# Performance work log

Measured on AMD Instinct MI355X. Metric: run time of the kernel, lower is better.

## Reference

```python
import jax, jax.numpy as jnp
import numpy as np


def _edt(fg):
    """Exact 2D Euclidean distance transform.

    fg: [B, H, W] bool, True = foreground. Returns, for every pixel, the
    Euclidean distance to the nearest background (False) pixel; 0 on
    background pixels. Matches scipy.ndimage.distance_transform_edt.
    Two-pass separable algorithm: exact 1D city-block distance along axis 1,
    then exact lower-envelope min along axis 2 via a scan over columns.
    """
    B, H, W = fg.shape
    BIG = jnp.float32(H + W)  # larger than any achievable distance
    bg = ~fg
    row_idx = jnp.arange(H, dtype=jnp.float32)[None, :, None]  # [1,H,1]

    def dist_to_prev_bg(bg_mask):
        # distance (along axis 1) to the most recent background pixel above
        last = jax.lax.cummax(jnp.where(bg_mask, row_idx, -BIG), axis=1)
        return row_idx - last

    d_up = dist_to_prev_bg(bg)
    d_down = jnp.flip(dist_to_prev_bg(jnp.flip(bg, axis=1)), axis=1)
    g = jnp.minimum(jnp.minimum(d_up, d_down), BIG)  # [B,H,W] 1D vertical dist
    g2 = g * g

    # Second pass: D2[b,h,x] = min_{x'} g2[b,h,x'] + (x - x')^2  (exact EDT^2)
    x = jnp.arange(W, dtype=jnp.float32)  # [W]

    def body(D2, inp):
        xp, g2col = inp  # scalar, [B,H]
        cand = g2col[:, :, None] + (x - xp) ** 2  # [B,H,W]
        return jnp.minimum(D2, cand), None

    D2_init = jnp.full((B, H, W), (2.0 * BIG) ** 2, dtype=jnp.float32)
    D2, _ = jax.lax.scan(body, D2_init, (x, jnp.moveaxis(g2, 2, 0)))
    return jnp.sqrt(D2)


def setup_inputs() -> dict:
    key = jax.random.key(0)
    k1, k2 = jax.random.split(key)
    B, C, H, W = 8, 4, 256, 256
    logits = jax.random.normal(k1, (B, C, H, W), dtype=jnp.float32)
    pred_softmax = jax.nn.softmax(logits, axis=1)
    mask = jax.random.randint(k2, (B, H, W), 0, C, dtype=jnp.int64)
    return {"pred_softmax": pred_softmax, "mask": mask}


def reference(pred_softmax, mask):
    B, C, H, W = pred_softmax.shape
    norm = np.float32(np.sqrt(H * H + W * W) + 1e-6)
    loss = jnp.float32(0.0)
    for c in range(1, C):  # small fixed number of classes
        fg = mask == c
        dist = _edt(fg) / norm  # [B,H,W]; all-zeros when class absent, as in ref
        loss = loss + jnp.mean(pred_softmax[:, c] * dist)
    return loss / max(C - 1, 1)
```

## Files before the change

### kernel.cpp

```cpp
#include <hip/hip_runtime.h>
#include <math.h>

#define B_    8
#define C_    4
#define H_    256
#define W_    256
#define NCLS  3
#define NROWS (NCLS * B_ * H_)
#define BIGVAL (1 << 26)

__global__ __launch_bounds__(256) void vert_g_kernel(const int* __restrict__ mask,
                                                     unsigned short* __restrict__ gbuf) {
    const int lane = threadIdx.x & 63;
    const int hc   = threadIdx.x >> 6;
    const int blk  = blockIdx.x;
    const int wt   = blk & 3;
    const int b    = (blk >> 2) & 7;
    const int c_i  = blk >> 5;
    const int cls  = c_i + 1;
    const int w    = (wt << 6) + lane;

    __shared__ int last_sh[4][64];
    __shared__ int first_sh[4][64];

    const int* mptr = mask + (b << 16) + (hc << 14) + w;
    int m[64];
    #pragma unroll
    for (int i = 0; i < 64; ++i) m[i] = mptr[i << 8];
    unsigned long long bg = 0ull;
    #pragma unroll
    for (int i = 0; i < 64; ++i)
        bg |= (unsigned long long)(m[i] != cls) << i;

    last_sh[hc][lane]  = bg ? ((hc << 6) + 63 - __builtin_clzll(bg)) : -512;
    first_sh[hc][lane] = bg ? ((hc << 6) + __builtin_ctzll(bg)) : (1 << 20);
    __syncthreads();

    int carry_up = -512;
    #pragma unroll
    for (int k = 0; k < 4; ++k)
        if (k < hc) carry_up = max(carry_up, last_sh[k][lane]);
    int carry_dn = 1 << 20;
    #pragma unroll
    for (int k = 0; k < 4; ++k)
        if (k > hc) carry_dn = min(carry_dn, first_sh[k][lane]);

    unsigned short* gout = gbuf + (((c_i << 3) + b) << 16) + (hc << 14) + w;
    #pragma unroll 4
    for (int i = 0; i < 64; ++i) {
        int h = (hc << 6) + i;
        unsigned long long le = bg & (~0ull >> (63 - i));
        int last = le ? ((hc << 6) + 63 - __builtin_clzll(le)) : carry_up;
        int du = h - last;
        unsigned long long ge = bg >> i;
        int first = ge ? (h + __builtin_ctzll(ge)) : carry_dn;
        int dd = first - h;
        int g = min(min(du, dd), 512);
        gout[i << 8] = (unsigned short)g;
    }
}

__global__ __launch_bounds__(256) void horiz_kernel(const unsigned short* __restrict__ gbuf,
                                                    const float* __restrict__ pred,
                                                    double* __restrict__ acc) {
    const int lane = threadIdx.x & 63;
    const int wv   = threadIdx.x >> 6;
    const int row  = blockIdx.x * 4 + wv;
    const int c_i  = row >> 11;
    const int b    = (row >> 8) & 7;
    const int h    = row & 255;
    const int cls  = c_i + 1;

    __shared__ __align__(16) int ext[4][512];

    const int x0 = lane << 2;
    const float* prow = pred + ((((b << 2) + cls) << 8) + h) * 256;
    float4 pv = *(const float4*)(prow + x0);
    ushort4 gv = *(const ushort4*)(gbuf + row * 256 + x0);

    int g0 = gv.x, g1 = gv.y, g2v = gv.z, g3 = gv.w;
    int q0 = g0 * g0, q1 = g1 * g1, q2 = g2v * g2v, q3 = g3 * g3;
    *(int4*)&ext[wv][128 + x0] = make_int4(q0, q1, q2, q3);
    ext[wv][lane]       = BIGVAL;
    ext[wv][64 + lane]  = BIGVAL;
    ext[wv][384 + lane] = BIGVAL;
    ext[wv][448 + lane] = BIGVAL;

    int gm = max(max(g0, g1), max(g2v, g3));
    #pragma unroll
    for (int off = 32; off > 0; off >>= 1) gm = max(gm, __shfl_xor(gm, off, 64));
    const int R = gm - 1;

    int D2[4] = { q0, q1, q2, q3 };
    const int* e = &ext[wv][128];

    if (R >= 120) {
        for (int xp = 0; xp < 256; ++xp) {
            int s = e[xp];
            #pragma unroll
            for (int j = 0; j < 4; ++j) {
                int d = (x0 + j) - xp;
                int cand = s + d * d;
                D2[j] = (cand < D2[j]) ? cand : D2[j];
            }
        }
    } else if (R >= 1) {
        for (int o = 1; o <= R; ++o) {
            int oo = o * o;
            #pragma unroll
            for (int j = 0; j < 4; ++j) {
                int xj = x0 + j;
                int c1 = e[xj + o];
                int c2 = e[xj - o];
                int cm = (c1 < c2) ? c1 : c2;
                int cand = cm + oo;
                D2[j] = (cand < D2[j]) ? cand : D2[j];
            }
        }
    }

    double sum = (double)(sqrtf((float)D2[0]) * pv.x)
               + (double)(sqrtf((float)D2[1]) * pv.y)
               + (double)(sqrtf((float)D2[2]) * pv.z)
               + (double)(sqrtf((float)D2[3]) * pv.w);
    #pragma unroll
    for (int off = 32; off > 0; off >>= 1) sum += __shfl_xor(sum, off, 64);
    if (lane == 0) acc[row] = sum;
}

__global__ __launch_bounds__(256) void final_kernel(const double* __restrict__ acc,
                                                    float* __restrict__ out) {
    const int t = threadIdx.x;
    __shared__ double wsum[4];
    double s = 0.0;
    #pragma unroll
    for (int i = 0; i < NROWS / 256; ++i) s += acc[t + i * 256];
    #pragma unroll
    for (int off = 32; off > 0; off >>= 1) s += __shfl_xor(s, off, 64);
    if ((t & 63) == 0) wsum[t >> 6] = s;
    __syncthreads();
    if (t == 0) {
        double total = wsum[0] + wsum[1] + wsum[2] + wsum[3];
        double nd = sqrt(131072.0) + 1e-6;
        double norm = (double)(float)nd;
        out[0] = (float)(total / norm / ((double)NCLS * (double)(B_ * H_ * W_)));
    }
}

extern "C" void kernel_launch(void* const* d_in, const int* in_sizes, int n_in,
                              void* d_out, int out_size, void* d_ws, size_t ws_size,
                              hipStream_t stream) {
    const float* pred = (const float*)d_in[0];
    const int*   mask = (const int*)d_in[1];
    float* out = (float*)d_out;

    char* ws = (char*)d_ws;
    double* acc = (double*)ws;
    unsigned short* gbuf = (unsigned short*)(ws + 65536);

    vert_g_kernel<<<NCLS * 8 * 4, 256, 0, stream>>>(mask, gbuf);
    horiz_kernel<<<NROWS / 4, 256, 0, stream>>>(gbuf, pred, acc);
    final_kernel<<<1, 256, 0, stream>>>(acc, out);
}
```

Measured before the change: 68.31 us.

## Fuse three kernels into one cooperative kernel with grid-wide syncs

Replaces the vertical-pass, horizontal-pass and final-reduction kernels with a single cooperative launch of 96 blocks, separated by grid.sync(). This removes two kernel launch gaps. The horizontal pass no longer uses 1536 blocks with one row per wave; each wave now processes 16 rows in batches with prefetched loads. The trade-off is far fewer waves on the GPU (384 waves), so latency hiding and parallelism for the horizontal stage are reduced, and grid.sync adds its own cost.

```diff
diff --git a/kernel.cpp b/kernel.cpp
--- a/kernel.cpp
+++ b/kernel.cpp
@@ -1,149 +1,172 @@
 #include <hip/hip_runtime.h>
+#include <hip/hip_cooperative_groups.h>
 #include <math.h>
+
+namespace cg = cooperative_groups;
 
 #define B_    8
 #define C_    4
 #define H_    256
 #define W_    256
 #define NCLS  3
-#define NROWS (NCLS * B_ * H_)
+#define NBLKC 96
 #define BIGVAL (1 << 26)
 
-__global__ __launch_bounds__(256) void vert_g_kernel(const int* __restrict__ mask,
-                                                     unsigned short* __restrict__ gbuf) {
-    const int lane = threadIdx.x & 63;
-    const int hc   = threadIdx.x >> 6;
+__global__ __launch_bounds__(256) void fused_coop(const int* __restrict__ mask,
+                                                  const float* __restrict__ pred,
+                                                  unsigned short* __restrict__ gbuf,
+                                                  double* __restrict__ part,
+                                                  float* __restrict__ out) {
+    cg::grid_group grid = cg::this_grid();
+    const int t    = threadIdx.x;
+    const int lane = t & 63;
+    const int wv   = t >> 6;
     const int blk  = blockIdx.x;
-    const int wt   = blk & 3;
-    const int b    = (blk >> 2) & 7;
-    const int c_i  = blk >> 5;
-    const int cls  = c_i + 1;
-    const int w    = (wt << 6) + lane;
 
     __shared__ int last_sh[4][64];
     __shared__ int first_sh[4][64];
+    __shared__ __align__(16) int ext[4][512];
+    __shared__ double bsum[4];
 
-    const int* mptr = mask + (b << 16) + (hc << 14) + w;
-    int m[64];
-    #pragma unroll
-    for (int i = 0; i < 64; ++i) m[i] = mptr[i << 8];
-    unsigned long long bg = 0ull;
-    #pragma unroll
-    for (int i = 0; i < 64; ++i)
-        bg |= (unsigned long long)(m[i] != cls) << i;
+    {
+        const int hc  = wv;
+        const int wt  = blk & 3;
+        const int b   = (blk >> 2) & 7;
+        const int c_i = blk >> 5;
+        const int cls = c_i + 1;
+        const int w   = (wt << 6) + lane;
 
-    last_sh[hc][lane]  = bg ? ((hc << 6) + 63 - __builtin_clzll(bg)) : -512;
-    first_sh[hc][lane] = bg ? ((hc << 6) + __builtin_ctzll(bg)) : (1 << 20);
-    __syncthreads();
+        const int* mptr = mask + (b << 16) + (hc << 14) + w;
+        int m[64];
+        #pragma unroll
+        for (int i = 0; i < 64; ++i) m[i] = mptr[i << 8];
+        unsigned long long bg = 0ull;
+        #pragma unroll
+        for (int i = 0; i < 64; ++i)
+            bg |= (unsigned long long)(m[i] != cls) << i;
 
-    int carry_up = -512;
-    #pragma unroll
-    for (int k = 0; k < 4; ++k)
-        if (k < hc) carry_up = max(carry_up, last_sh[k][lane]);
-    int carry_dn = 1 << 20;
-    #pragma unroll
-    for (int k = 0; k < 4; ++k)
-        if (k > hc) carry_dn = min(carry_dn, first_sh[k][lane]);
+        last_sh[hc][lane]  = bg ? ((hc << 6) + 63 - __builtin_clzll(bg)) : -512;
+        first_sh[hc][lane] = bg ? ((hc << 6) + __builtin_ctzll(bg)) : (1 << 20);
+        __syncthreads();
 
-    unsigned short* gout = gbuf + (((c_i << 3) + b) << 16) + (hc << 14) + w;
-    #pragma unroll 4
-    for (int i = 0; i < 64; ++i) {
-        int h = (hc << 6) + i;
-        unsigned long long le = bg & (~0ull >> (63 - i));
-        int last = le ? ((hc << 6) + 63 - __builtin_clzll(le)) : carry_up;
-        int du = h - last;
-        unsigned long long ge = bg >> i;
-        int first = ge ? (h + __builtin_ctzll(ge)) : carry_dn;
-        int dd = first - h;
-        int g = min(min(du, dd), 512);
-        gout[i << 8] = (unsigned short)g;
-    }
-}
+        int carry_up = -512;
+        #pragma unroll
+        for (int k = 0; k < 4; ++k)
+            if (k < hc) carry_up = max(carry_up, last_sh[k][lane]);
+        int carry_dn = 1 << 20;
+        #pragma unroll
+        for (int k = 0; k < 4; ++k)
+            if (k > hc) carry_dn = min(carry_dn, first_sh[k][lane]);
 
-__global__ __launch_bounds__(256) void horiz_kernel(const unsigned short* __restrict__ gbuf,
-                                                    const float* __restrict__ pred,
-                                                    double* __restrict__ acc) {
-    const int lane = threadIdx.x & 63;
-    const int wv   = threadIdx.x >> 6;
-    const int row  = blockIdx.x * 4 + wv;
-    const int c_i  = row >> 11;
-    const int b    = (row >> 8) & 7;
-    const int h    = row & 255;
-    const int cls  = c_i + 1;
-
-    __shared__ __align__(16) int ext[4][512];
-
-    const int x0 = lane << 2;
-    const float* prow = pred + ((((b << 2) + cls) << 8) + h) * 256;
-    float4 pv = *(const float4*)(prow + x0);
-    ushort4 gv = *(const ushort4*)(gbuf + row * 256 + x0);
-
-    int g0 = gv.x, g1 = gv.y, g2v = gv.z, g3 = gv.w;
-    int q0 = g0 * g0, q1 = g1 * g1, q2 = g2v * g2v, q3 = g3 * g3;
-    *(int4*)&ext[wv][128 + x0] = make_int4(q0, q1, q2, q3);
-    ext[wv][lane]       = BIGVAL;
-    ext[wv][64 + lane]  = BIGVAL;
-    ext[wv][384 + lane] = BIGVAL;
-    ext[wv][448 + lane] = BIGVAL;
-
-    int gm = max(max(g0, g1), max(g2v, g3));
-    #pragma unroll
-    for (int off = 32; off > 0; off >>= 1) gm = max(gm, __shfl_xor(gm, off, 64));
-    const int R = gm - 1;
-
-    int D2[4] = { q0, q1, q2, q3 };
-    const int* e = &ext[wv][128];
-
-    if (R >= 120) {
-        for (int xp = 0; xp < 256; ++xp) {
-            int s = e[xp];
-            #pragma unroll
-            for (int j = 0; j < 4; ++j) {
-                int d = (x0 + j) - xp;
-                int cand = s + d * d;
-                D2[j] = (cand < D2[j]) ? cand : D2[j];
-            }
-        }
-    } else if (R >= 1) {
-        for (int o = 1; o <= R; ++o) {
-            int oo = o * o;
-            #pragma unroll
-            for (int j = 0; j < 4; ++j) {
-                int xj = x0 + j;
-                int c1 = e[xj + o];
-                int c2 = e[xj - o];
-                int cm = (c1 < c2) ? c1 : c2;
-                int cand = cm + oo;
-                D2[j] = (cand < D2[j]) ? cand : D2[j];
-            }
+        unsigned short* gout = gbuf + (((c_i << 3) + b) << 16) + (hc << 14) + w;
+        #pragma unroll 4
+        for (int i = 0; i < 64; ++i) {
+            int h = (hc << 6) + i;
+            unsigned long long le = bg & (~0ull >> (63 - i));
+            int last = le ? ((hc << 6) + 63 - __builtin_clzll(le)) : carry_up;
+            int du = h - last;
+            unsigned long long ge = bg >> i;
+            int first = ge ? (h + __builtin_ctzll(ge)) : carry_dn;
+            int dd = first - h;
+            int g = min(min(du, dd), 512);
+            gout[i << 8] = (unsigned short)g;
         }
     }
 
-    double sum = (double)(sqrtf((float)D2[0]) * pv.x)
-               + (double)(sqrtf((float)D2[1]) * pv.y)
-               + (double)(sqrtf((float)D2[2]) * pv.z)
-               + (double)(sqrtf((float)D2[3]) * pv.w);
-    #pragma unroll
-    for (int off = 32; off > 0; off >>= 1) sum += __shfl_xor(sum, off, 64);
-    if (lane == 0) acc[row] = sum;
-}
+    grid.sync();
 
-__global__ __launch_bounds__(256) void final_kernel(const double* __restrict__ acc,
-                                                    float* __restrict__ out) {
-    const int t = threadIdx.x;
-    __shared__ double wsum[4];
-    double s = 0.0;
-    #pragma unroll
-    for (int i = 0; i < NROWS / 256; ++i) s += acc[t + i * 256];
-    #pragma unroll
-    for (int off = 32; off > 0; off >>= 1) s += __shfl_xor(s, off, 64);
-    if ((t & 63) == 0) wsum[t >> 6] = s;
-    __syncthreads();
-    if (t == 0) {
-        double total = wsum[0] + wsum[1] + wsum[2] + wsum[3];
-        double nd = sqrt(131072.0) + 1e-6;
-        double norm = (double)(float)nd;
-        out[0] = (float)(total / norm / ((double)NCLS * (double)(B_ * H_ * W_)));
+    double sum = 0.0;
+    {
+        ext[wv][lane]       = BIGVAL;
+        ext[wv][64 + lane]  = BIGVAL;
+        ext[wv][384 + lane] = BIGVAL;
+        ext[wv][448 + lane] = BIGVAL;
+
+        const int gi  = blk * 4 + wv;
+        const int c_i = gi >> 7;
+        const int b   = (gi >> 4) & 7;
+        const int h0  = (gi & 15) << 4;
+        const int cls = c_i + 1;
+        const int x0  = lane << 2;
+
+        const unsigned short* grow = gbuf + (((c_i << 3) + b) << 16) + (h0 << 8) + x0;
+        const float*          prow = pred + (((b << 2) + cls) << 16) + (h0 << 8) + x0;
+
+        #pragma unroll 1
+        for (int batch = 0; batch < 2; ++batch) {
+            ushort4 gv[8];
+            float4  pv[8];
+            #pragma unroll
+            for (int rr = 0; rr < 8; ++rr) {
+                int ro = ((batch << 3) + rr) << 8;
+                gv[rr] = *(const ushort4*)(grow + ro);
+                pv[rr] = *(const float4*)(prow + ro);
+            }
+            #pragma unroll 1
+            for (int rr = 0; rr < 8; ++rr) {
+                int g0 = gv[rr].x, g1 = gv[rr].y, g2v = gv[rr].z, g3 = gv[rr].w;
+                int q0 = g0 * g0, q1 = g1 * g1, q2 = g2v * g2v, q3 = g3 * g3;
+                *(int4*)&ext[wv][128 + x0] = make_int4(q0, q1, q2, q3);
+
+                int gm = max(max(g0, g1), max(g2v, g3));
+                #pragma unroll
+                for (int off = 32; off > 0; off >>= 1)
+                    gm = max(gm, __shfl_xor(gm, off, 64));
+                const int R = gm - 1;
+
+                int D2[4] = { q0, q1, q2, q3 };
+                const int* e = &ext[wv][128];
+
+                if (R >= 120) {
+                    for (int xp = 0; xp < 256; ++xp) {
+                        int s = e[xp];
+                        #pragma unroll
+                        for (int j = 0; j < 4; ++j) {
+                            int d = (x0 + j) - xp;
+                            int cand = s + d * d;
+                            D2[j] = (cand < D2[j]) ? cand : D2[j];
+                        }
+                    }
+                } else if (R >= 1) {
+                    for (int o = 1; o <= R; ++o) {
+                        int oo = o * o;
+                        #pragma unroll
+                        for (int j = 0; j < 4; ++j) {
+                            int xj = x0 + j;
+                            int c1 = e[xj + o];
+                            int c2 = e[xj - o];
+                            int cm = (c1 < c2) ? c1 : c2;
+                            int cand = cm + oo;
+                            D2[j] = (cand < D2[j]) ? cand : D2[j];
+                        }
+                    }
+                }
+
+                sum += (double)(sqrtf((float)D2[0]) * pv[rr].x)
+                     + (double)(sqrtf((float)D2[1]) * pv[rr].y)
+                     + (double)(sqrtf((float)D2[2]) * pv[rr].z)
+                     + (double)(sqrtf((float)D2[3]) * pv[rr].w);
+            }
+        }
+        #pragma unroll
+        for (int off = 32; off > 0; off >>= 1) sum += __shfl_xor(sum, off, 64);
+        if (lane == 0) part[gi] = sum;
+    }
+
+    grid.sync();
+
+    if (blk == 0) {
+        double s = part[t] + ((t < 128) ? part[t + 256] : 0.0);
+        #pragma unroll
+        for (int off = 32; off > 0; off >>= 1) s += __shfl_xor(s, off, 64);
+        if ((t & 63) == 0) bsum[t >> 6] = s;
+        __syncthreads();
+        if (t == 0) {
+            double total = bsum[0] + bsum[1] + bsum[2] + bsum[3];
+            double nd = sqrt(131072.0) + 1e-6;
+            double norm = (double)(float)nd;
+            out[0] = (float)(total / norm / ((double)NCLS * (double)(B_ * H_ * W_)));
+        }
     }
 }
 
@@ -155,10 +178,10 @@
     float* out = (float*)d_out;
 
     char* ws = (char*)d_ws;
-    double* acc = (double*)ws;
+    double* part = (double*)ws;
     unsigned short* gbuf = (unsigned short*)(ws + 65536);
 
-    vert_g_kernel<<<NCLS * 8 * 4, 256, 0, stream>>>(mask, gbuf);
-    horiz_kernel<<<NROWS / 4, 256, 0, stream>>>(gbuf, pred, acc);
-    final_kernel<<<1, 256, 0, stream>>>(acc, out);
+    void* args[] = { (void*)&mask, (void*)&pred, (void*)&gbuf, (void*)&part, (void*)&out };
+    hipLaunchCooperativeKernel((const void*)fused_coop, dim3(NBLKC), dim3(256),
+                               args, 0, stream);
 }
```

Result: slower. 117.6 us (+72.2%).
